# Optimization experiments

Measured on AMD Instinct MI355X. Metric: run time of the kernel, lower is better.

## Reference

```python
import jax, jax.numpy as jnp
import numpy as np

DIM = 128
N = 16          # num_nodes
B = 8           # batch size
H = 4096        # MLP hidden width
SLOPE = 0.01    # LeakyReLU default negative slope
PI_ITERS = 50   # fixed-iteration power iteration (max_error=1e-5 regime)


def setup_inputs() -> dict:
    key = jax.random.key(0)
    ks = jax.random.split(key, 12)
    w = lambda k, shape: jax.random.normal(k, shape, jnp.float32) * 0.02
    return {
        "nodes_embeddings": jax.random.normal(ks[0], (B, N, DIM), jnp.float32),
        "graphs_embeddings": jax.random.normal(ks[1], (B, DIM), jnp.float32),
        "Ts": jax.random.uniform(ks[2], (B, N, N), jnp.float32),
        "W1": w(ks[3], (2 * DIM, H)), "b1": jnp.zeros((H,), jnp.float32),
        "W2": w(ks[4], (H, H)),       "b2": jnp.zeros((H,), jnp.float32),
        "W3": w(ks[5], (H, H)),       "b3": jnp.zeros((H,), jnp.float32),
        "W4": w(ks[6], (H, N * N)),   "b4": jnp.zeros((N * N,), jnp.float32),
    }


def _mlp(x, W1, b1, W2, b2, W3, b3, W4, b4):
    # Linear -> LeakyReLU -> (Dropout=eval identity), x3, then Linear -> LeakyReLU -> Sigmoid
    h = jax.nn.leaky_relu(x @ W1 + b1, SLOPE)
    h = jax.nn.leaky_relu(h @ W2 + b2, SLOPE)
    h = jax.nn.leaky_relu(h @ W3 + b3, SLOPE)
    return jax.nn.sigmoid(jax.nn.leaky_relu(h @ W4 + b4, SLOPE))


def _power_iteration(A):
    # A: (..., n, n), entries > 0 (sigmoid outputs) -> dominant (Perron) eigenvector.
    v0 = jnp.ones(A.shape[:-1], A.dtype)
    def step(v, _):
        w = jnp.einsum('...ij,...j->...i', A, v)
        v = w / jnp.linalg.norm(w, axis=-1, keepdims=True)
        return v, None
    v, _ = jax.lax.scan(step, v0, None, length=PI_ITERS)
    return v


def reference(nodes_embeddings, graphs_embeddings, Ts, W1, b1, W2, b2, W3, b3, W4, b4):
    Bn, Nn, D = nodes_embeddings.shape
    P = Nn * Nn
    pair = jnp.arange(P)
    s_ids = pair // Nn  # outer loop index s
    t_ids = pair % Nn   # inner loop index t

    embT = jnp.transpose(nodes_embeddings, (1, 0, 2))      # (N, B, D)
    s_all = embT[s_ids]                                    # (P, B, D)
    t_all = embT[t_ids]                                    # (P, B, D)
    # Faithful to torch.stack([s, t]).view(batch, 2*dim): a flat reinterpretation,
    # NOT a per-row concat. stack axis=1 -> (P, 2, B, D) then reshape -> (P, B, 2D).
    x = jnp.stack([s_all, t_all], axis=1).reshape(P, Bn, 2 * D)

    pol = _mlp(x.reshape(P * Bn, 2 * D), W1, b1, W2, b2, W3, b3, W4, b4)
    pol = pol.reshape(P, Bn, Nn, Nn)                       # predecessor prob matrices

    vec = _power_iteration(pol)                            # (P, B, N)
    v_src = vec[pair, :, s_ids]                            # (P, B) eigenvector[src]
    T_pair = jnp.transpose(Ts.reshape(Bn, P), (1, 0))      # (P, B), pair order s*N+t

    contrib = vec / v_src[:, :, None] * T_pair[:, :, None]  # (P, B, N)
    return jnp.sum(contrib, axis=0)                         # (B, N) == Cs
```

## Files before the change

kernel.cpp:

```cpp
#include <hip/hip_runtime.h>

typedef unsigned short u16;
typedef unsigned int u32;
typedef __attribute__((ext_vector_type(8))) short short8;
typedef __attribute__((ext_vector_type(4))) float f32x4;

__device__ __forceinline__ u16 f2bf(float f) {
    unsigned u = __float_as_uint(f);
    return (u16)((u + 0x7FFFu + ((u >> 16) & 1u)) >> 16);
}
__device__ __forceinline__ u32 pack2(float a, float b) {
    return ((u32)f2bf(b) << 16) | (u32)f2bf(a);
}

#define ROR1 0x121
#define ROR2 0x122
#define ROR4 0x124
#define ROR8 0x128
template<int C> __device__ __forceinline__ float dppf(float x) {
    int i = __float_as_int(x);
    return __int_as_float(__builtin_amdgcn_update_dpp(i, i, C, 0xF, 0xF, false));
}
template<int C> __device__ __forceinline__ int dppi(int x) {
    return __builtin_amdgcn_update_dpp(x, x, C, 0xF, 0xF, false);
}

template<int SRC, int EPI>
__global__ __launch_bounds__(256, 2) void k_gemm(
    const u16* __restrict__ A, const float* __restrict__ emb,
    const float* __restrict__ W, const float* __restrict__ bias,
    float* __restrict__ Cp, u16* __restrict__ Ho, float* __restrict__ Po,
    int N, int kchunk)
{
    __shared__ __align__(16) u16 Alds[64][40];
    __shared__ __align__(16) u32 Wlds[16 * 132];
    int tid = threadIdx.x;
    int wv = tid >> 6, lane = tid & 63, c = lane & 15, g = lane >> 4;
    int c0 = blockIdx.x * 128;
    int k0 = blockIdx.y * kchunk;
    int nit = kchunk >> 5;

    int ar = tid >> 2, aseg = tid & 3;
    int kp = tid >> 4, cbase = (tid & 15) * 8;

    f32x4 acc[8];
    #pragma unroll
    for (int n = 0; n < 8; ++n) acc[n] = (f32x4){0.f, 0.f, 0.f, 0.f};

    auto loadA = [&](int kc, uint4& av) {
        if (SRC == 0) {
            av = *(const uint4*)(A + (size_t)ar * 4096 + k0 + kc + aseg * 8);
        } else {
            int e0 = kc + aseg * 8;
            int b = 2 * (ar & 3) + (e0 >> 7), d = e0 & 127;
            const float4* s = (const float4*)(emb + (b * 16 + (ar >> 2)) * 128 + d);
            float4 f0 = s[0], f1 = s[1];
            av.x = pack2(f0.x, f0.y); av.y = pack2(f0.z, f0.w);
            av.z = pack2(f1.x, f1.y); av.w = pack2(f1.z, f1.w);
        }
    };
    auto loadW = [&](int kc, float4& q0, float4& q1, float4& q2, float4& q3) {
        const float* s0 = W + (size_t)(k0 + kc + 2 * kp) * N + c0 + cbase;
        q0 = ((const float4*)s0)[0]; q1 = ((const float4*)s0)[1];
        const float* s1 = s0 + N;
        q2 = ((const float4*)s1)[0]; q3 = ((const float4*)s1)[1];
    };
    auto stage = [&](const uint4& av, const float4& q0, const float4& q1,
                     const float4& q2, const float4& q3) {
        *(uint4*)&Alds[ar][aseg * 8] = av;
        uint4 w0, w1;
        w0.x = pack2(q0.x, q2.x); w0.y = pack2(q0.y, q2.y);
        w0.z = pack2(q0.z, q2.z); w0.w = pack2(q0.w, q2.w);
        w1.x = pack2(q1.x, q3.x); w1.y = pack2(q1.y, q3.y);
        w1.z = pack2(q1.z, q3.z); w1.w = pack2(q1.w, q3.w);
        uint4* wd = (uint4*)&Wlds[kp * 132 + cbase];
        wd[0] = w0; wd[1] = w1;
    };
    auto compute = [&]() {
        short8 a8 = *(const short8*)&Alds[wv * 16 + c][g * 8];
        #pragma unroll
        for (int n = 0; n < 8; ++n) {
            int base = n * 16 + c;
            union { u32 u[4]; short8 s; } bb;
            bb.u[0] = Wlds[(g * 4 + 0) * 132 + base];
            bb.u[1] = Wlds[(g * 4 + 1) * 132 + base];
            bb.u[2] = Wlds[(g * 4 + 2) * 132 + base];
            bb.u[3] = Wlds[(g * 4 + 3) * 132 + base];
            acc[n] = __builtin_amdgcn_mfma_f32_16x16x32_bf16(a8, bb.s, acc[n], 0, 0, 0);
        }
    };

    uint4 avA, avB;
    float4 qA0, qA1, qA2, qA3, qB0, qB1, qB2, qB3;
    loadA(0, avA);  loadW(0, qA0, qA1, qA2, qA3);
    loadA(32, avB); loadW(32, qB0, qB1, qB2, qB3);

    for (int it = 0; it < nit; it += 2) {
        stage(avA, qA0, qA1, qA2, qA3);
        __syncthreads();
        if (it + 2 < nit) {
            loadA((it + 2) * 32, avA);
            loadW((it + 2) * 32, qA0, qA1, qA2, qA3);
        }
        compute();
        __syncthreads();

        stage(avB, qB0, qB1, qB2, qB3);
        __syncthreads();
        if (it + 3 < nit) {
            loadA((it + 3) * 32, avB);
            loadW((it + 3) * 32, qB0, qB1, qB2, qB3);
        }
        compute();
        __syncthreads();
    }

    #pragma unroll
    for (int n = 0; n < 8; ++n) {
        #pragma unroll
        for (int rr = 0; rr < 4; ++rr) {
            int grow = wv * 16 + g * 4 + rr;
            int gcol = c0 + n * 16 + c;
            float v = acc[n][rr];
            if (EPI == 0) {
                Cp[(size_t)blockIdx.y * 64 * N + (size_t)grow * N + gcol] = v;
            } else {
                v += bias[gcol];
                v = (v >= 0.f) ? v : 0.01f * v;
                if (EPI == 1) Ho[(size_t)grow * N + gcol] = f2bf(v);
                else          Po[(size_t)grow * N + gcol] = 1.0f / (1.0f + __expf(-v));
            }
        }
    }
}

__global__ void k_reduce(const float* __restrict__ Cp, const float* __restrict__ bias,
                         u16* __restrict__ Hb, float* __restrict__ Pf,
                         int N, int ksplit, int mode)
{
    int idx = blockIdx.x * 256 + threadIdx.x;
    int col = idx & (N - 1);
    float s = bias[col];
    #pragma unroll 4
    for (int k = 0; k < ksplit; ++k) s += Cp[(size_t)k * 64 * N + idx];
    float a = (s >= 0.f) ? s : 0.01f * s;
    if (mode == 0) Hb[idx] = f2bf(a);
    else           Pf[idx] = 1.0f / (1.0f + __expf(-a));
}

__global__ __launch_bounds__(1024) void k_power_out(
    const float* __restrict__ pol,
    const float* __restrict__ Ts,
    float* __restrict__ out)
{
    __shared__ float pol_lds[16384];
    __shared__ float w_lds[64][16];
    __shared__ float Ts_lds[2048];
    __shared__ float Cmat[8][16];

    int tid = threadIdx.x;
    int m = tid >> 4, r = tid & 15;

    {
        const float4* p4 = (const float4*)(pol + tid * 16);
        float4* q4 = (float4*)&pol_lds[tid * 16];
        q4[0] = p4[0]; q4[1] = p4[1]; q4[2] = p4[2]; q4[3] = p4[3];
    }
    Ts_lds[tid] = Ts[tid];
    Ts_lds[tid + 1024] = Ts[tid + 1024];
    __syncthreads();

    float Mr[8], Ms[8];
    {
        int mb = m * 256 + r * 16;
        int idx = r;
        #pragma unroll
        for (int k = 0; k < 8; ++k) { Mr[k] = pol_lds[mb + idx]; idx = dppi<ROR1>(idx); }
        #pragma unroll
        for (int k = 0; k < 8; ++k) { Ms[k] = pol_lds[mb + idx]; idx = dppi<ROR1>(idx); }
    }

    float v = 1.0f;
    #pragma unroll 1
    for (int it = 0; it < 50; ++it) {
        float va = v, vb = dppf<ROR8>(v);
        float w = 0.f, w2 = 0.f;
        #pragma unroll
        for (int k = 0; k < 8; ++k) {
            w  = fmaf(Mr[k], va, w);
            w2 = fmaf(Ms[k], vb, w2);
            if (k < 7) { va = dppf<ROR1>(va); vb = dppf<ROR1>(vb); }
        }
        w += w2;
        if ((it & 7) == 7) {
            float s = w;
            s += dppf<ROR8>(s); s += dppf<ROR4>(s);
            s += dppf<ROR2>(s); s += dppf<ROR1>(s);
            w *= 1.0f / s;
        }
        v = w;
    }
    w_lds[m][r] = v;
    __syncthreads();

    if (tid < 128) {
        int b = tid >> 4, x = tid & 15;
        float s = 0.f;
        if (b < 4) {
            const float* row = &Ts_lds[(b * 16 + x) * 16];
            #pragma unroll
            for (int t = 0; t < 16; ++t) s += row[t];
        } else {
            int j = b - 4;
            #pragma unroll
            for (int si = 0; si < 16; ++si)
                s += Ts_lds[(b * 16 + si) * 16 + x] / w_lds[x * 4 + j][si];
        }
        Cmat[b][x] = s;
    }
    __syncthreads();

    if (tid < 128) {
        int b = tid >> 4, n = tid & 15;
        float o = 0.f;
        if (b < 4) {
            #pragma unroll
            for (int si = 0; si < 16; ++si) {
                const float* wr = w_lds[si * 4 + b];
                o += wr[n] / wr[si] * Cmat[b][si];
            }
        } else {
            int j = b - 4;
            #pragma unroll
            for (int t = 0; t < 16; ++t)
                o += w_lds[t * 4 + j][n] * Cmat[b][t];
        }
        out[b * 16 + n] = o;
    }
}

extern "C" void kernel_launch(void* const* d_in, const int* in_sizes, int n_in,
                              void* d_out, int out_size, void* d_ws, size_t ws_size,
                              hipStream_t stream)
{
    const float* emb = (const float*)d_in[0];
    const float* Ts  = (const float*)d_in[2];
    const float* W1  = (const float*)d_in[3];  const float* b1 = (const float*)d_in[4];
    const float* W2  = (const float*)d_in[5];  const float* b2 = (const float*)d_in[6];
    const float* W3  = (const float*)d_in[7];  const float* b3 = (const float*)d_in[8];
    const float* W4  = (const float*)d_in[9];  const float* b4 = (const float*)d_in[10];
    float* outp = (float*)d_out;

    char* ws = (char*)d_ws;
    u16*   Ha  = (u16*)(ws + 0);
    u16*   Hb  = (u16*)(ws + 524288);
    float* pol = (float*)(ws + 1048576);
    float* Cp  = (float*)(ws + 1114112);

    size_t need16 = (size_t)1114112 + (size_t)16 * 1048576;
    int KS = (ws_size >= need16) ? 16 : 8;
    int kchunk = 4096 / KS;

    k_gemm<1, 1><<<dim3(32, 1), 256, 0, stream>>>(
        nullptr, emb, W1, b1, nullptr, Ha, nullptr, 4096, 256);

    k_gemm<0, 0><<<dim3(32, KS), 256, 0, stream>>>(
        Ha, nullptr, W2, nullptr, Cp, nullptr, nullptr, 4096, kchunk);
    k_reduce<<<1024, 256, 0, stream>>>(Cp, b2, Hb, nullptr, 4096, KS, 0);

    k_gemm<0, 0><<<dim3(32, KS), 256, 0, stream>>>(
        Hb, nullptr, W3, nullptr, Cp, nullptr, nullptr, 4096, kchunk);
    k_reduce<<<1024, 256, 0, stream>>>(Cp, b3, Ha, nullptr, 4096, KS, 0);

    k_gemm<0, 0><<<dim3(2, 32), 256, 0, stream>>>(
        Ha, nullptr, W4, nullptr, Cp, nullptr, nullptr, 256, 128);
    k_reduce<<<64, 256, 0, stream>>>(Cp, b4, nullptr, pol, 256, 32, 1);

    k_power_out<<<1, 1024, 0, stream>>>(pol, Ts, outp);

    (void)in_sizes; (void)n_in; (void)out_size; (void)ws_size;
}
```

Measured before the change: 79.62 us.

## Halve GEMM column tile, store split-K partials in bf16, vectorize reduce

The GEMM column tile shrinks from 128 to 64, doubling the grid so more blocks run across CUs, and launch bounds are raised to 4 blocks per CU. Split-K partial sums are now written in bf16 instead of fp32, halving partial-buffer traffic. The reduce kernel reads 8 bf16 partials per thread with 16-byte loads. The trade-off is some precision loss from rounding partials to bf16 before summing, and each A tile is reloaded twice as often across column blocks.

```diff
diff --git a/kernel.cpp b/kernel.cpp
--- a/kernel.cpp
+++ b/kernel.cpp
@@ -12,6 +12,8 @@
 __device__ __forceinline__ u32 pack2(float a, float b) {
     return ((u32)f2bf(b) << 16) | (u32)f2bf(a);
 }
+__device__ __forceinline__ float bfhi(u32 w) { return __uint_as_float(w & 0xFFFF0000u); }
+__device__ __forceinline__ float bflo(u32 w) { return __uint_as_float(w << 16); }
 
 #define ROR1 0x121
 #define ROR2 0x122
@@ -26,26 +28,26 @@
 }
 
 template<int SRC, int EPI>
-__global__ __launch_bounds__(256, 2) void k_gemm(
+__global__ __launch_bounds__(256, 4) void k_gemm(
     const u16* __restrict__ A, const float* __restrict__ emb,
     const float* __restrict__ W, const float* __restrict__ bias,
-    float* __restrict__ Cp, u16* __restrict__ Ho, float* __restrict__ Po,
+    u16* __restrict__ Cp, u16* __restrict__ Ho,
     int N, int kchunk)
 {
     __shared__ __align__(16) u16 Alds[64][40];
-    __shared__ __align__(16) u32 Wlds[16 * 132];
+    __shared__ __align__(16) u32 Wlds[16 * 66];
     int tid = threadIdx.x;
     int wv = tid >> 6, lane = tid & 63, c = lane & 15, g = lane >> 4;
-    int c0 = blockIdx.x * 128;
+    int c0 = blockIdx.x * 64;
     int k0 = blockIdx.y * kchunk;
     int nit = kchunk >> 5;
 
     int ar = tid >> 2, aseg = tid & 3;
-    int kp = tid >> 4, cbase = (tid & 15) * 8;
-
-    f32x4 acc[8];
-    #pragma unroll
-    for (int n = 0; n < 8; ++n) acc[n] = (f32x4){0.f, 0.f, 0.f, 0.f};
+    int kp = tid >> 4, cbase = (tid & 15) * 4;
+
+    f32x4 acc[4];
+    #pragma unroll
+    for (int n = 0; n < 4; ++n) acc[n] = (f32x4){0.f, 0.f, 0.f, 0.f};
 
     auto loadA = [&](int kc, uint4& av) {
         if (SRC == 0) {
@@ -59,93 +61,93 @@
             av.z = pack2(f1.x, f1.y); av.w = pack2(f1.z, f1.w);
         }
     };
-    auto loadW = [&](int kc, float4& q0, float4& q1, float4& q2, float4& q3) {
+    auto loadW = [&](int kc, float4& q0, float4& q1) {
         const float* s0 = W + (size_t)(k0 + kc + 2 * kp) * N + c0 + cbase;
-        q0 = ((const float4*)s0)[0]; q1 = ((const float4*)s0)[1];
-        const float* s1 = s0 + N;
-        q2 = ((const float4*)s1)[0]; q3 = ((const float4*)s1)[1];
-    };
-    auto stage = [&](const uint4& av, const float4& q0, const float4& q1,
-                     const float4& q2, const float4& q3) {
+        q0 = *(const float4*)s0;
+        q1 = *(const float4*)(s0 + N);
+    };
+    auto stage = [&](const uint4& av, const float4& q0, const float4& q1) {
         *(uint4*)&Alds[ar][aseg * 8] = av;
-        uint4 w0, w1;
-        w0.x = pack2(q0.x, q2.x); w0.y = pack2(q0.y, q2.y);
-        w0.z = pack2(q0.z, q2.z); w0.w = pack2(q0.w, q2.w);
-        w1.x = pack2(q1.x, q3.x); w1.y = pack2(q1.y, q3.y);
-        w1.z = pack2(q1.z, q3.z); w1.w = pack2(q1.w, q3.w);
-        uint4* wd = (uint4*)&Wlds[kp * 132 + cbase];
-        wd[0] = w0; wd[1] = w1;
+        uint4 w0;
+        w0.x = pack2(q0.x, q1.x); w0.y = pack2(q0.y, q1.y);
+        w0.z = pack2(q0.z, q1.z); w0.w = pack2(q0.w, q1.w);
+        *(uint4*)&Wlds[kp * 66 + cbase] = w0;
     };
     auto compute = [&]() {
         short8 a8 = *(const short8*)&Alds[wv * 16 + c][g * 8];
         #pragma unroll
-        for (int n = 0; n < 8; ++n) {
+        for (int n = 0; n < 4; ++n) {
             int base = n * 16 + c;
             union { u32 u[4]; short8 s; } bb;
-            bb.u[0] = Wlds[(g * 4 + 0) * 132 + base];
-            bb.u[1] = Wlds[(g * 4 + 1) * 132 + base];
-            bb.u[2] = Wlds[(g * 4 + 2) * 132 + base];
-            bb.u[3] = Wlds[(g * 4 + 3) * 132 + base];
+            bb.u[0] = Wlds[(g * 4 + 0) * 66 + base];
+            bb.u[1] = Wlds[(g * 4 + 1) * 66 + base];
+            bb.u[2] = Wlds[(g * 4 + 2) * 66 + base];
+            bb.u[3] = Wlds[(g * 4 + 3) * 66 + base];
             acc[n] = __builtin_amdgcn_mfma_f32_16x16x32_bf16(a8, bb.s, acc[n], 0, 0, 0);
         }
     };
 
     uint4 avA, avB;
-    float4 qA0, qA1, qA2, qA3, qB0, qB1, qB2, qB3;
-    loadA(0, avA);  loadW(0, qA0, qA1, qA2, qA3);
-    loadA(32, avB); loadW(32, qB0, qB1, qB2, qB3);
+    float4 qA0, qA1, qB0, qB1;
+    loadA(0, avA);  loadW(0, qA0, qA1);
+    loadA(32, avB); loadW(32, qB0, qB1);
 
     for (int it = 0; it < nit; it += 2) {
-        stage(avA, qA0, qA1, qA2, qA3);
-        __syncthreads();
-        if (it + 2 < nit) {
-            loadA((it + 2) * 32, avA);
-            loadW((it + 2) * 32, qA0, qA1, qA2, qA3);
-        }
+        stage(avA, qA0, qA1);
+        __syncthreads();
+        if (it + 2 < nit) { loadA((it + 2) * 32, avA); loadW((it + 2) * 32, qA0, qA1); }
         compute();
         __syncthreads();
 
-        stage(avB, qB0, qB1, qB2, qB3);
-        __syncthreads();
-        if (it + 3 < nit) {
-            loadA((it + 3) * 32, avB);
-            loadW((it + 3) * 32, qB0, qB1, qB2, qB3);
-        }
+        stage(avB, qB0, qB1);
+        __syncthreads();
+        if (it + 3 < nit) { loadA((it + 3) * 32, avB); loadW((it + 3) * 32, qB0, qB1); }
         compute();
         __syncthreads();
     }
 
     #pragma unroll
-    for (int n = 0; n < 8; ++n) {
+    for (int n = 0; n < 4; ++n) {
         #pragma unroll
         for (int rr = 0; rr < 4; ++rr) {
             int grow = wv * 16 + g * 4 + rr;
             int gcol = c0 + n * 16 + c;
             float v = acc[n][rr];
             if (EPI == 0) {
-                Cp[(size_t)blockIdx.y * 64 * N + (size_t)grow * N + gcol] = v;
+                Cp[((size_t)blockIdx.y * 64 + grow) * N + gcol] = f2bf(v);
             } else {
                 v += bias[gcol];
                 v = (v >= 0.f) ? v : 0.01f * v;
-                if (EPI == 1) Ho[(size_t)grow * N + gcol] = f2bf(v);
-                else          Po[(size_t)grow * N + gcol] = 1.0f / (1.0f + __expf(-v));
+                Ho[(size_t)grow * N + gcol] = f2bf(v);
             }
         }
     }
 }
 
-__global__ void k_reduce(const float* __restrict__ Cp, const float* __restrict__ bias,
-                         u16* __restrict__ Hb, float* __restrict__ Pf,
-                         int N, int ksplit, int mode)
-{
-    int idx = blockIdx.x * 256 + threadIdx.x;
-    int col = idx & (N - 1);
-    float s = bias[col];
-    #pragma unroll 4
-    for (int k = 0; k < ksplit; ++k) s += Cp[(size_t)k * 64 * N + idx];
-    float a = (s >= 0.f) ? s : 0.01f * s;
-    if (mode == 0) Hb[idx] = f2bf(a);
-    else           Pf[idx] = 1.0f / (1.0f + __expf(-a));
+__global__ __launch_bounds__(256) void k_reduce(
+    const u16* __restrict__ Cp, const float* __restrict__ bias,
+    u16* __restrict__ Hb, float* __restrict__ Pf,
+    int N, int ksplit, int mode)
+{
+    int e0 = (blockIdx.x * 256 + threadIdx.x) * 8;
+    float s[8];
+    #pragma unroll
+    for (int j = 0; j < 8; ++j) s[j] = 0.f;
+    for (int k = 0; k < ksplit; ++k) {
+        uint4 w = *(const uint4*)(Cp + (size_t)k * 64 * N + e0);
+        s[0] += bflo(w.x); s[1] += bfhi(w.x);
+        s[2] += bflo(w.y); s[3] += bfhi(w.y);
+        s[4] += bflo(w.z); s[5] += bfhi(w.z);
+        s[6] += bflo(w.w); s[7] += bfhi(w.w);
+    }
+    int colb = e0 & (N - 1);
+    #pragma unroll
+    for (int j = 0; j < 8; ++j) {
+        float a = s[j] + bias[colb + j];
+        a = (a >= 0.f) ? a : 0.01f * a;
+        if (mode == 0) Hb[e0 + j] = f2bf(a);
+        else           Pf[e0 + j] = 1.0f / (1.0f + __expf(-a));
+    }
 }
 
 __global__ __launch_bounds__(1024) void k_power_out(
@@ -255,26 +257,26 @@
     u16*   Ha  = (u16*)(ws + 0);
     u16*   Hb  = (u16*)(ws + 524288);
     float* pol = (float*)(ws + 1048576);
-    float* Cp  = (float*)(ws + 1114112);
-
-    size_t need16 = (size_t)1114112 + (size_t)16 * 1048576;
+    u16*   Cp  = (u16*)(ws + 1114112);
+
+    size_t need16 = (size_t)1114112 + (size_t)16 * 524288;
     int KS = (ws_size >= need16) ? 16 : 8;
     int kchunk = 4096 / KS;
 
-    k_gemm<1, 1><<<dim3(32, 1), 256, 0, stream>>>(
-        nullptr, emb, W1, b1, nullptr, Ha, nullptr, 4096, 256);
-
-    k_gemm<0, 0><<<dim3(32, KS), 256, 0, stream>>>(
-        Ha, nullptr, W2, nullptr, Cp, nullptr, nullptr, 4096, kchunk);
-    k_reduce<<<1024, 256, 0, stream>>>(Cp, b2, Hb, nullptr, 4096, KS, 0);
-
-    k_gemm<0, 0><<<dim3(32, KS), 256, 0, stream>>>(
-        Hb, nullptr, W3, nullptr, Cp, nullptr, nullptr, 4096, kchunk);
-    k_reduce<<<1024, 256, 0, stream>>>(Cp, b3, Ha, nullptr, 4096, KS, 0);
-
-    k_gemm<0, 0><<<dim3(2, 32), 256, 0, stream>>>(
-        Ha, nullptr, W4, nullptr, Cp, nullptr, nullptr, 256, 128);
-    k_reduce<<<64, 256, 0, stream>>>(Cp, b4, nullptr, pol, 256, 32, 1);
+    k_gemm<1, 1><<<dim3(64, 1), 256, 0, stream>>>(
+        nullptr, emb, W1, b1, nullptr, Ha, 4096, 256);
+
+    k_gemm<0, 0><<<dim3(64, KS), 256, 0, stream>>>(
+        Ha, nullptr, W2, nullptr, Cp, nullptr, 4096, kchunk);
+    k_reduce<<<128, 256, 0, stream>>>(Cp, b2, Hb, nullptr, 4096, KS, 0);
+
+    k_gemm<0, 0><<<dim3(64, KS), 256, 0, stream>>>(
+        Hb, nullptr, W3, nullptr, Cp, nullptr, 4096, kchunk);
+    k_reduce<<<128, 256, 0, stream>>>(Cp, b3, Ha, nullptr, 4096, KS, 0);
+
+    k_gemm<0, 0><<<dim3(4, 32), 256, 0, stream>>>(
+        Ha, nullptr, W4, nullptr, Cp, nullptr, 256, 128);
+    k_reduce<<<8, 256, 0, stream>>>(Cp, b4, nullptr, pol, 256, 32, 1);
 
     k_power_out<<<1, 1024, 0, stream>>>(pol, Ts, outp);
 
```

Result: slower. 91.62 us (+15.1%).

## Fuse split-K reduction into GEMM via last-block atomic counter with bf16 partials

Applied to the files above, without the earlier changes.

Removes the three separate split-K reduce kernels by having each GEMM block write bf16 partials and bump a per-column-tile atomic counter. The last block to arrive for a tile sums the partials and applies bias, LeakyReLU and bf16 or sigmoid output. This saves launch overhead and halves partial-sum traffic by storing partials in bf16 instead of fp32. In exchange it adds a memset, thread fences, and extra rounding error in the partial sums, and the final reduction runs serially in one block per tile.

```diff
diff --git a/kernel.cpp b/kernel.cpp
--- a/kernel.cpp
+++ b/kernel.cpp
@@ -12,6 +12,8 @@
 __device__ __forceinline__ u32 pack2(float a, float b) {
     return ((u32)f2bf(b) << 16) | (u32)f2bf(a);
 }
+__device__ __forceinline__ float bfhi(u32 w) { return __uint_as_float(w & 0xFFFF0000u); }
+__device__ __forceinline__ float bflo(u32 w) { return __uint_as_float(w << 16); }
 
 #define ROR1 0x121
 #define ROR2 0x122
@@ -25,25 +27,19 @@
     return __builtin_amdgcn_update_dpp(x, x, C, 0xF, 0xF, false);
 }
 
-template<int SRC, int EPI>
-__global__ __launch_bounds__(256, 2) void k_gemm(
+template<int SRC>
+__device__ __forceinline__ void gemm_core(
     const u16* __restrict__ A, const float* __restrict__ emb,
-    const float* __restrict__ W, const float* __restrict__ bias,
-    float* __restrict__ Cp, u16* __restrict__ Ho, float* __restrict__ Po,
-    int N, int kchunk)
-{
-    __shared__ __align__(16) u16 Alds[64][40];
-    __shared__ __align__(16) u32 Wlds[16 * 132];
-    int tid = threadIdx.x;
+    const float* __restrict__ W, int N, int kchunk, int c0, int k0,
+    char* smem, int tid, f32x4* acc)
+{
+    u16 (*Alds)[40] = (u16(*)[40])smem;
+    u32* Wlds = (u32*)(smem + 5120);
     int wv = tid >> 6, lane = tid & 63, c = lane & 15, g = lane >> 4;
-    int c0 = blockIdx.x * 128;
-    int k0 = blockIdx.y * kchunk;
     int nit = kchunk >> 5;
-
     int ar = tid >> 2, aseg = tid & 3;
     int kp = tid >> 4, cbase = (tid & 15) * 8;
 
-    f32x4 acc[8];
     #pragma unroll
     for (int n = 0; n < 8; ++n) acc[n] = (f32x4){0.f, 0.f, 0.f, 0.f};
 
@@ -98,54 +94,96 @@
     for (int it = 0; it < nit; it += 2) {
         stage(avA, qA0, qA1, qA2, qA3);
         __syncthreads();
-        if (it + 2 < nit) {
-            loadA((it + 2) * 32, avA);
-            loadW((it + 2) * 32, qA0, qA1, qA2, qA3);
-        }
+        if (it + 2 < nit) { loadA((it + 2) * 32, avA); loadW((it + 2) * 32, qA0, qA1, qA2, qA3); }
         compute();
         __syncthreads();
 
         stage(avB, qB0, qB1, qB2, qB3);
         __syncthreads();
-        if (it + 3 < nit) {
-            loadA((it + 3) * 32, avB);
-            loadW((it + 3) * 32, qB0, qB1, qB2, qB3);
-        }
+        if (it + 3 < nit) { loadA((it + 3) * 32, avB); loadW((it + 3) * 32, qB0, qB1, qB2, qB3); }
         compute();
         __syncthreads();
     }
-
+}
+
+__global__ __launch_bounds__(256, 2) void k_l1(
+    const float* __restrict__ emb, const float* __restrict__ W,
+    const float* __restrict__ bias, u16* __restrict__ Ho)
+{
+    __shared__ __align__(16) char smem[13568];
+    int tid = threadIdx.x;
+    f32x4 acc[8];
+    gemm_core<1>(nullptr, emb, W, 4096, 256, blockIdx.x * 128, 0, smem, tid, acc);
+    int wv = tid >> 6, lane = tid & 63, c = lane & 15, g = lane >> 4;
+    int c0 = blockIdx.x * 128;
     #pragma unroll
     for (int n = 0; n < 8; ++n) {
         #pragma unroll
         for (int rr = 0; rr < 4; ++rr) {
             int grow = wv * 16 + g * 4 + rr;
             int gcol = c0 + n * 16 + c;
-            float v = acc[n][rr];
-            if (EPI == 0) {
-                Cp[(size_t)blockIdx.y * 64 * N + (size_t)grow * N + gcol] = v;
-            } else {
-                v += bias[gcol];
-                v = (v >= 0.f) ? v : 0.01f * v;
-                if (EPI == 1) Ho[(size_t)grow * N + gcol] = f2bf(v);
-                else          Po[(size_t)grow * N + gcol] = 1.0f / (1.0f + __expf(-v));
-            }
-        }
-    }
-}
-
-__global__ void k_reduce(const float* __restrict__ Cp, const float* __restrict__ bias,
-                         u16* __restrict__ Hb, float* __restrict__ Pf,
-                         int N, int ksplit, int mode)
-{
-    int idx = blockIdx.x * 256 + threadIdx.x;
-    int col = idx & (N - 1);
-    float s = bias[col];
-    #pragma unroll 4
-    for (int k = 0; k < ksplit; ++k) s += Cp[(size_t)k * 64 * N + idx];
-    float a = (s >= 0.f) ? s : 0.01f * s;
-    if (mode == 0) Hb[idx] = f2bf(a);
-    else           Pf[idx] = 1.0f / (1.0f + __expf(-a));
+            float v = acc[n][rr] + bias[gcol];
+            v = (v >= 0.f) ? v : 0.01f * v;
+            Ho[(size_t)grow * 4096 + gcol] = f2bf(v);
+        }
+    }
+}
+
+template<int EPI>
+__global__ __launch_bounds__(256, 2) void k_gemm_fix(
+    const u16* __restrict__ A, const float* __restrict__ W,
+    const float* __restrict__ bias, u16* __restrict__ Cp16,
+    int* __restrict__ cnt, u16* __restrict__ Ho, float* __restrict__ Po,
+    int N, int kchunk, int KS)
+{
+    __shared__ __align__(16) char smem[13568];
+    __shared__ int s_last;
+    int tid = threadIdx.x;
+    int cx = blockIdx.x, ky = blockIdx.y;
+    int c0 = cx * 128;
+    f32x4 acc[8];
+    gemm_core<0>(A, nullptr, W, N, kchunk, c0, ky * kchunk, smem, tid, acc);
+
+    u16* slice = Cp16 + (size_t)(cx * KS + ky) * 8192;
+    int wv = tid >> 6, lane = tid & 63, c = lane & 15, g = lane >> 4;
+    #pragma unroll
+    for (int n = 0; n < 8; ++n) {
+        #pragma unroll
+        for (int rr = 0; rr < 4; ++rr) {
+            int grow = wv * 16 + g * 4 + rr;
+            slice[grow * 128 + n * 16 + c] = f2bf(acc[n][rr]);
+        }
+    }
+    __threadfence();
+    __syncthreads();
+    if (tid == 0) s_last = (atomicAdd(&cnt[cx], 1) == KS - 1);
+    __syncthreads();
+    if (!s_last) return;
+    __threadfence();
+
+    const u16* base = Cp16 + (size_t)cx * KS * 8192;
+    #pragma unroll
+    for (int j = 0; j < 4; ++j) {
+        int e0 = (tid + j * 256) * 8;
+        float s[8];
+        #pragma unroll
+        for (int q = 0; q < 8; ++q) s[q] = 0.f;
+        for (int k = 0; k < KS; ++k) {
+            uint4 w4 = *(const uint4*)(base + (size_t)k * 8192 + e0);
+            s[0] += bflo(w4.x); s[1] += bfhi(w4.x);
+            s[2] += bflo(w4.y); s[3] += bfhi(w4.y);
+            s[4] += bflo(w4.z); s[5] += bfhi(w4.z);
+            s[6] += bflo(w4.w); s[7] += bfhi(w4.w);
+        }
+        int row = e0 >> 7, colin = e0 & 127;
+        #pragma unroll
+        for (int q = 0; q < 8; ++q) {
+            float a = s[q] + bias[c0 + colin + q];
+            a = (a >= 0.f) ? a : 0.01f * a;
+            if (EPI == 0) Ho[(size_t)row * N + c0 + colin + q] = f2bf(a);
+            else          Po[(size_t)row * N + c0 + colin + q] = 1.0f / (1.0f + __expf(-a));
+        }
+    }
 }
 
 __global__ __launch_bounds__(1024) void k_power_out(
@@ -207,9 +245,8 @@
         int b = tid >> 4, x = tid & 15;
         float s = 0.f;
         if (b < 4) {
-            const float* row = &Ts_lds[(b * 16 + x) * 16];
             #pragma unroll
-            for (int t = 0; t < 16; ++t) s += row[t];
+            for (int t = 0; t < 16; ++t) s += Ts_lds[(b * 16 + x) * 16 + t];
         } else {
             int j = b - 4;
             #pragma unroll
@@ -255,26 +292,25 @@
     u16*   Ha  = (u16*)(ws + 0);
     u16*   Hb  = (u16*)(ws + 524288);
     float* pol = (float*)(ws + 1048576);
-    float* Cp  = (float*)(ws + 1114112);
-
-    size_t need16 = (size_t)1114112 + (size_t)16 * 1048576;
+    int*   cnt = (int*)(ws + 1114112);
+    u16*   Cp  = (u16*)(ws + 1118208);
+
+    size_t need16 = (size_t)1118208 + (size_t)16 * 524288;
     int KS = (ws_size >= need16) ? 16 : 8;
     int kchunk = 4096 / KS;
 
-    k_gemm<1, 1><<<dim3(32, 1), 256, 0, stream>>>(
-        nullptr, emb, W1, b1, nullptr, Ha, nullptr, 4096, 256);
-
-    k_gemm<0, 0><<<dim3(32, KS), 256, 0, stream>>>(
-        Ha, nullptr, W2, nullptr, Cp, nullptr, nullptr, 4096, kchunk);
-    k_reduce<<<1024, 256, 0, stream>>>(Cp, b2, Hb, nullptr, 4096, KS, 0);
-
-    k_gemm<0, 0><<<dim3(32, KS), 256, 0, stream>>>(
-        Hb, nullptr, W3, nullptr, Cp, nullptr, nullptr, 4096, kchunk);
-    k_reduce<<<1024, 256, 0, stream>>>(Cp, b3, Ha, nullptr, 4096, KS, 0);
-
-    k_gemm<0, 0><<<dim3(2, 32), 256, 0, stream>>>(
-        Ha, nullptr, W4, nullptr, Cp, nullptr, nullptr, 256, 128);
-    k_reduce<<<64, 256, 0, stream>>>(Cp, b4, nullptr, pol, 256, 32, 1);
+    hipMemsetAsync(cnt, 0, 4096, stream);
+
+    k_l1<<<dim3(32, 1), 256, 0, stream>>>(emb, W1, b1, Ha);
+
+    k_gemm_fix<0><<<dim3(32, KS), 256, 0, stream>>>(
+        Ha, W2, b2, Cp, cnt + 0, Hb, nullptr, 4096, kchunk, KS);
+
+    k_gemm_fix<0><<<dim3(32, KS), 256, 0, stream>>>(
+        Hb, W3, b3, Cp, cnt + 32, Ha, nullptr, 4096, kchunk, KS);
+
+    k_gemm_fix<1><<<dim3(2, 32), 256, 0, stream>>>(
+        Ha, W4, b4, Cp, cnt + 64, nullptr, pol, 256, 128, 32);
 
     k_power_out<<<1, 1024, 0, stream>>>(pol, Ts, outp);
 
```

After: 280.2 us. 3.52x slower.
